# Kernel optimization log

Measured on AMD Instinct MI355X. Metric: run time of the kernel, lower is better.

The kernel has to match this reference:

```python
import jax, jax.numpy as jnp
import numpy as np

ALPHA = 0.1  # LeakyReLU negative slope
F_OUT = 128

def _leaky(x):
    return jnp.where(x >= 0, x, ALPHA * x)

def setup_inputs() -> dict:
    key = jax.random.key(0)
    ks = jax.random.split(key, 12)
    B, N, F_IN = 4, 4096, 128
    q = jax.random.normal(ks[0], (B, N, F_IN), jnp.float32)
    k = jax.random.normal(ks[1], (B, N, F_IN), jnp.float32)
    v = jax.random.normal(ks[2], (B, N, F_IN), jnp.float32)
    adj = jax.random.randint(ks[3], (B, N, N), 0, 2, jnp.int32)
    s = 1.0 / np.sqrt(F_IN)
    Wq_w = jax.random.uniform(ks[4], (F_OUT, F_IN), jnp.float32, -s, s)
    Wq_b = jax.random.uniform(ks[5], (F_OUT,), jnp.float32, -s, s)
    Wk_w = jax.random.uniform(ks[6], (F_OUT, F_IN), jnp.float32, -s, s)
    Wk_b = jax.random.uniform(ks[7], (F_OUT,), jnp.float32, -s, s)
    Wv_w = jax.random.uniform(ks[8], (F_OUT, F_IN), jnp.float32, -s, s)
    Wv_b = jax.random.uniform(ks[9], (F_OUT,), jnp.float32, -s, s)
    # xavier_uniform with gain=1.414 on (2F,1)
    lim = 1.414 * np.sqrt(6.0 / (2 * F_OUT + 1))
    a = jax.random.uniform(ks[10], (2 * F_OUT, 1), jnp.float32, -lim, lim)
    so = 1.0 / np.sqrt(F_OUT)
    Wo_w = jax.random.uniform(ks[11], (F_OUT, F_OUT), jnp.float32, -so, so)
    return {"q": q, "k": k, "v": v, "adj": adj, "Wq_w": Wq_w, "Wq_b": Wq_b,
            "Wk_w": Wk_w, "Wk_b": Wk_b, "Wv_w": Wv_w, "Wv_b": Wv_b,
            "a": a, "Wo_w": Wo_w}

def reference(q, k, v, adj, Wq_w, Wq_b, Wk_w, Wk_b, Wv_w, Wv_b, a, Wo_w):
    qp = q @ Wq_w.T + Wq_b                      # (B,N,F)
    kp = k @ Wk_w.T + Wk_b
    vp = v @ Wv_w.T + Wv_b
    Wh1 = qp @ a[:F_OUT]                        # (B,N,1)
    Wh2 = kp @ a[F_OUT:]                        # (B,N,1)
    e = _leaky(Wh1 + jnp.swapaxes(Wh2, 1, 2))   # (B,N,N)
    e = jnp.where(adj > 0, e, jnp.float32(-1e9))
    att = jax.nn.softmax(e, axis=-1)
    h = jnp.einsum('bnm,bmf->bnf', att, vp)     # (B,N,F)
    return _leaky(h @ Wo_w.T)
```

## Files before the change

### kernel.cpp

```cpp
#include <hip/hip_runtime.h>


constexpr int B = 4, N = 4096, F = 128;
constexpr int BN = B * N;
constexpr int BK = 64;
constexpr int SPLITS = 4;
constexpr int JC = N / SPLITS;
constexpr int NIT = JC / BK;
#define ALPHA 0.1f

using float4v = __attribute__((ext_vector_type(4))) float;
using short8 = __attribute__((ext_vector_type(8))) short;

__device__ __forceinline__ float leaky(float x) { return x >= 0.f ? x : ALPHA * x; }
__device__ __forceinline__ unsigned short f2bf(float x) {
    unsigned u = __float_as_uint(x);
    u = (u + 0x7FFFu + ((u >> 16) & 1u)) >> 16;
    return (unsigned short)u;
}
__device__ __forceinline__ unsigned pack_bf2(float lo, float hi) {
    unsigned a = __float_as_uint(lo), b2 = __float_as_uint(hi);
    a = a + 0x7FFFu + ((a >> 16) & 1u);
    b2 = b2 + 0x7FFFu + ((b2 >> 16) & 1u);
    return __builtin_amdgcn_perm(b2, a, 0x07060302u);
}

__global__ void k_prep(const float* __restrict__ Wq_w, const float* __restrict__ Wq_b,
                       const float* __restrict__ Wk_w, const float* __restrict__ Wk_b,
                       const float* __restrict__ a, float* __restrict__ c1,
                       float* __restrict__ c2, float* __restrict__ d12) {
    __shared__ float as[2 * F];
    __shared__ float red[2 * F];
    int t = threadIdx.x;
    as[t] = a[t];
    __syncthreads();
    int f = t & 127;
    const float* W = (t < F) ? Wq_w : Wk_w;
    const float* ao = (t < F) ? as : as + F;
    float s = 0.f;
#pragma unroll 8
    for (int o = 0; o < F; o++) s = fmaf(W[o * F + f], ao[o], s);
    if (t < F) c1[f] = s; else c2[f] = s;
    red[t] = (t < F) ? Wq_b[f] * as[f] : Wk_b[f] * as[F + f];
    __syncthreads();
    for (int st = 64; st > 0; st >>= 1) {
        if (f < st) red[t] += red[t + st];
        __syncthreads();
    }
    if (t == 0) d12[0] = red[0];
    if (t == F) d12[1] = red[F];
}

__global__ void k_wh(const float* __restrict__ q, const float* __restrict__ k,
                     const float* __restrict__ c1, const float* __restrict__ c2,
                     const float* __restrict__ d12,
                     float* __restrict__ Wh1, float* __restrict__ Wh2) {
    __shared__ float c1s[F], c2s[F];
    int t = threadIdx.x;
    if (t < F) c1s[t] = c1[t]; else c2s[t - F] = c2[t - F];
    __syncthreads();
    int row = blockIdx.x * 8 + (t >> 5);
    int lane = t & 31;
    float4 q4 = reinterpret_cast<const float4*>(q)[row * 32 + lane];
    float4 k4 = reinterpret_cast<const float4*>(k)[row * 32 + lane];
    float s1 = q4.x * c1s[lane * 4 + 0] + q4.y * c1s[lane * 4 + 1] +
               q4.z * c1s[lane * 4 + 2] + q4.w * c1s[lane * 4 + 3];
    float s2 = k4.x * c2s[lane * 4 + 0] + k4.y * c2s[lane * 4 + 1] +
               k4.z * c2s[lane * 4 + 2] + k4.w * c2s[lane * 4 + 3];
    for (int m = 16; m > 0; m >>= 1) { s1 += __shfl_xor(s1, m); s2 += __shfl_xor(s2, m); }
    if (lane == 0) { Wh1[row] = s1 + d12[0]; Wh2[row] = s2 + d12[1]; }
}

__global__ void k_max2(const float* __restrict__ Wh2, float* __restrict__ M2) {
    int b = blockIdx.x, t = threadIdx.x;
    float m = -1e30f;
    for (int i = t; i < N; i += 256) m = fmaxf(m, Wh2[b * N + i]);
    __shared__ float red[256];
    red[t] = m;
    __syncthreads();
    for (int s = 128; s > 0; s >>= 1) { if (t < s) red[t] = fmaxf(red[t], red[t + s]); __syncthreads(); }
    if (t == 0) M2[b] = red[0];
}

__global__ void k_tab(const float* __restrict__ Wh1, const float* __restrict__ Wh2,
                      const float* __restrict__ M2,
                      float* __restrict__ P1, float* __restrict__ Q1,
                      float* __restrict__ P2, float* __restrict__ Q2) {
    int i = blockIdx.x * 256 + threadIdx.x;
    int b = i >> 12;
    float w1 = Wh1[i], w2 = Wh2[i];
    float mi = leaky(w1 + M2[b]);
    P1[i] = __expf(w1 - mi);
    Q1[i] = __expf(ALPHA * w1 - mi);
    P2[i] = __expf(w2);
    Q2[i] = __expf(ALPHA * w2);
}

__global__ __launch_bounds__(256) void k_vp(const float* __restrict__ v,
                                            const float* __restrict__ Wv_w,
                                            const float* __restrict__ Wv_b,
                                            unsigned short* __restrict__ vpT) {
    __shared__ float vs[32][F];
    __shared__ float Ws[F][129];
    __shared__ unsigned short ts[F][40];
    int t = threadIdx.x;
    int row0g = blockIdx.x * 32;
    int b = row0g >> 12;
    int row0 = row0g & (N - 1);
    {
        const float4* src = reinterpret_cast<const float4*>(v + row0g * F);
        float4* dst = reinterpret_cast<float4*>(&vs[0][0]);
#pragma unroll
        for (int u = 0; u < 4; u++) dst[u * 256 + t] = src[u * 256 + t];
    }
    {
        const float4* src = reinterpret_cast<const float4*>(Wv_w);
#pragma unroll
        for (int u = 0; u < 16; u++) {
            int unit = u * 256 + t;
            int r = unit >> 5, s = unit & 31;
            float4 val = src[unit];
            Ws[r][s * 4 + 0] = val.x; Ws[r][s * 4 + 1] = val.y;
            Ws[r][s * 4 + 2] = val.z; Ws[r][s * 4 + 3] = val.w;
        }
    }
    int f = t & 127, g = t >> 7;
    float bias = Wv_b[f];
    __syncthreads();
    float acc[16];
#pragma unroll
    for (int r = 0; r < 16; r++) acc[r] = bias;
    for (int kk = 0; kk < F; kk++) {
        float wk = Ws[f][kk];
#pragma unroll
        for (int r = 0; r < 16; r++) acc[r] = fmaf(vs[g * 16 + r][kk], wk, acc[r]);
    }
#pragma unroll
    for (int r = 0; r < 16; r++) ts[f][g * 16 + r] = f2bf(acc[r]);
    __syncthreads();
    int fr = t >> 1, hseg = t & 1;
    uint4 d0 = *reinterpret_cast<uint4*>(&ts[fr][hseg * 16]);
    uint4 d1 = *reinterpret_cast<uint4*>(&ts[fr][hseg * 16 + 8]);
    unsigned short* dst = vpT + ((size_t)(b * F + fr) * N + row0 + hseg * 16);
    *reinterpret_cast<uint4*>(dst) = d0;
    *reinterpret_cast<uint4*>(dst + 8) = d1;
}

__global__ __launch_bounds__(256, 2) void k_attn(
    const unsigned short* __restrict__ vpT, const int* __restrict__ adj,
    const float* __restrict__ Wh1, const float* __restrict__ P1, const float* __restrict__ Q1,
    const float* __restrict__ P2, const float* __restrict__ Q2, const float* __restrict__ Wh2,
    float* __restrict__ h_part, float* __restrict__ den_part) {
    __shared__ __align__(16) unsigned short bs[2][F][72];
    __shared__ __align__(16) float sP2[JC], sQ2[JC], sW2[JC];
    int t = threadIdx.x;
    int idx = blockIdx.x;
    int split = idx & 3;
    int tile = (idx >> 2) & 31;
    int b = idx >> 7;
    int i0 = tile * 128;
    int jb0 = split * JC;
    int widx = t >> 6, lane = t & 63, m = lane & 15, q = lane >> 4;
    int r0 = i0 + widx * 32;

    {
        reinterpret_cast<float4*>(sP2)[t] = reinterpret_cast<const float4*>(P2 + b * N + jb0)[t];
        reinterpret_cast<float4*>(sQ2)[t] = reinterpret_cast<const float4*>(Q2 + b * N + jb0)[t];
        reinterpret_cast<float4*>(sW2)[t] = reinterpret_cast<const float4*>(Wh2 + b * N + jb0)[t];
    }

    int gi0 = b * N + r0 + m;
    int gi1 = gi0 + 16;
    float p1a = P1[gi0], q1a = Q1[gi0], t1a = -Wh1[gi0];
    float p1b = P1[gi1], q1b = Q1[gi1], t1b = -Wh1[gi1];

    const unsigned short* vb = vpT + (size_t)b * F * N + jb0;
    const int* adjbase = adj + (size_t)gi0 * N + jb0 + q * 8;

    uint4 sreg[4];
    int4 aregA[8], aregB[8];

    auto load_stage = [&](int it) {
#pragma unroll
        for (int u = 0; u < 4; u++) {
            int unit = u * 256 + t;
            int r = unit >> 3, s = unit & 7;
            sreg[u] = *reinterpret_cast<const uint4*>(vb + (size_t)r * N + it * BK + s * 8);
        }
    };
    auto write_stage = [&](int pb) {
#pragma unroll
        for (int u = 0; u < 4; u++) {
            int unit = u * 256 + t;
            int r = unit >> 3, s = unit & 7;
            *reinterpret_cast<uint4*>(&bs[pb][r][s * 8]) = sreg[u];
        }
    };
    auto load_adj = [&](int it, int4* ar) {
#pragma unroll
        for (int rt = 0; rt < 2; rt++)
#pragma unroll
            for (int kh = 0; kh < 2; kh++) {
                const int* p = adjbase + (size_t)rt * 16 * N + it * BK + kh * 32;
                ar[(rt * 2 + kh) * 2 + 0] = *reinterpret_cast<const int4*>(p);
                ar[(rt * 2 + kh) * 2 + 1] = *reinterpret_cast<const int4*>(p + 4);
            }
    };

    float4v acc0[8], acc1[8];
#pragma unroll
    for (int nt = 0; nt < 8; nt++) {
        acc0[nt] = (float4v){0.f, 0.f, 0.f, 0.f};
        acc1[nt] = (float4v){0.f, 0.f, 0.f, 0.f};
    }
    float den0 = 0.f, den1 = 0.f;

    auto gen_af = [&](const int4& a0, const int4& a1, const float4& x2a, const float4& x2b,
                      const float4& p2a, const float4& p2b, const float4& q2a, const float4& q2b,
                      float p1, float q1, float t1, float& den) -> short8 {
        float w0 = a0.x ? ((x2a.x >= t1) ? p1 * p2a.x : q1 * q2a.x) : 0.f;
        float w1 = a0.y ? ((x2a.y >= t1) ? p1 * p2a.y : q1 * q2a.y) : 0.f;
        float w2 = a0.z ? ((x2a.z >= t1) ? p1 * p2a.z : q1 * q2a.z) : 0.f;
        float w3 = a0.w ? ((x2a.w >= t1) ? p1 * p2a.w : q1 * q2a.w) : 0.f;
        float w4 = a1.x ? ((x2b.x >= t1) ? p1 * p2b.x : q1 * q2b.x) : 0.f;
        float w5 = a1.y ? ((x2b.y >= t1) ? p1 * p2b.y : q1 * q2b.y) : 0.f;
        float w6 = a1.z ? ((x2b.z >= t1) ? p1 * p2b.z : q1 * q2b.z) : 0.f;
        float w7 = a1.w ? ((x2b.w >= t1) ? p1 * p2b.w : q1 * q2b.w) : 0.f;
        den += ((w0 + w1) + (w2 + w3)) + ((w4 + w5) + (w6 + w7));
        union { short8 s; uint4 u; } r;
        r.u.x = pack_bf2(w0, w1); r.u.y = pack_bf2(w2, w3);
        r.u.z = pack_bf2(w4, w5); r.u.w = pack_bf2(w6, w7);
        return r.s;
    };

    auto body = [&](int it, int4* cur, int4* nxt, int pb) {
        if (it + 1 < NIT) {
            load_stage(it + 1);
            load_adj(it + 1, nxt);
        }
#pragma unroll
        for (int kh = 0; kh < 2; kh++) {
            int jl = it * BK + kh * 32 + q * 8;
            float4 x2a = *reinterpret_cast<const float4*>(&sW2[jl]);
            float4 x2b = *reinterpret_cast<const float4*>(&sW2[jl + 4]);
            float4 p2a = *reinterpret_cast<const float4*>(&sP2[jl]);
            float4 p2b = *reinterpret_cast<const float4*>(&sP2[jl + 4]);
            float4 q2a = *reinterpret_cast<const float4*>(&sQ2[jl]);
            float4 q2b = *reinterpret_cast<const float4*>(&sQ2[jl + 4]);
            short8 af0 = gen_af(cur[kh * 2 + 0], cur[kh * 2 + 1], x2a, x2b, p2a, p2b, q2a, q2b,
                                p1a, q1a, t1a, den0);
            short8 af1 = gen_af(cur[(2 + kh) * 2 + 0], cur[(2 + kh) * 2 + 1], x2a, x2b, p2a, p2b,
                                q2a, q2b, p1b, q1b, t1b, den1);
#pragma unroll
            for (int nt = 0; nt < 8; nt++) {
                short8 bf = *reinterpret_cast<const short8*>(&bs[pb][nt * 16 + m][kh * 32 + q * 8]);
                acc0[nt] = __builtin_amdgcn_mfma_f32_16x16x32_bf16(af0, bf, acc0[nt], 0, 0, 0);
                acc1[nt] = __builtin_amdgcn_mfma_f32_16x16x32_bf16(af1, bf, acc1[nt], 0, 0, 0);
            }
        }
        if (it + 1 < NIT) write_stage(pb ^ 1);
        __syncthreads();
    };

    load_stage(0);
    load_adj(0, aregA);
    write_stage(0);
    __syncthreads();

#pragma unroll 1
    for (int ith = 0; ith < NIT / 2; ith++) {
        body(ith * 2 + 0, aregA, aregB, 0);
        body(ith * 2 + 1, aregB, aregA, 1);
    }

    den0 += __shfl_xor(den0, 16); den0 += __shfl_xor(den0, 32);
    den1 += __shfl_xor(den1, 16); den1 += __shfl_xor(den1, 32);
    float* dp = den_part + (size_t)split * BN;
    if (q == 0) { dp[gi0] = den0; dp[gi1] = den1; }
    float* hp = h_part + (size_t)split * BN * F;
    int orow0 = b * N + r0 + q * 4;
#pragma unroll
    for (int nt = 0; nt < 8; nt++)
#pragma unroll
        for (int r = 0; r < 4; r++) {
            hp[(size_t)(orow0 + r) * F + nt * 16 + m] = acc0[nt][r];
            hp[(size_t)(orow0 + 16 + r) * F + nt * 16 + m] = acc1[nt][r];
        }
}

__global__ __launch_bounds__(256) void k_out(const float* __restrict__ h_part,
                                             const float* __restrict__ den_part,
                                             const float* __restrict__ Wo_w,
                                             float* __restrict__ out) {
    __shared__ float hs[32][F];
    __shared__ float Ws[F][129];
    int t = threadIdx.x;
    int row0 = blockIdx.x * 32;
    {
        const float4* src = reinterpret_cast<const float4*>(Wo_w);
#pragma unroll
        for (int u = 0; u < 16; u++) {
            int unit = u * 256 + t;
            int r = unit >> 5, s = unit & 31;
            float4 val = src[unit];
            Ws[r][s * 4 + 0] = val.x; Ws[r][s * 4 + 1] = val.y;
            Ws[r][s * 4 + 2] = val.z; Ws[r][s * 4 + 3] = val.w;
        }
    }
#pragma unroll
    for (int u = 0; u < 4; u++) {
        int unit = u * 256 + t;
        int r = unit >> 5, s = unit & 31;
        size_t off = (size_t)(row0 + r) * F + s * 4;
        float4 h0 = *reinterpret_cast<const float4*>(h_part + off);
        float4 h1 = *reinterpret_cast<const float4*>(h_part + (size_t)BN * F + off);
        float4 h2 = *reinterpret_cast<const float4*>(h_part + (size_t)2 * BN * F + off);
        float4 h3 = *reinterpret_cast<const float4*>(h_part + (size_t)3 * BN * F + off);
        float dsum = den_part[row0 + r] + den_part[BN + row0 + r] +
                     den_part[2 * BN + row0 + r] + den_part[3 * BN + row0 + r];
        float inv = 1.f / dsum;
        hs[r][s * 4 + 0] = (h0.x + h1.x + h2.x + h3.x) * inv;
        hs[r][s * 4 + 1] = (h0.y + h1.y + h2.y + h3.y) * inv;
        hs[r][s * 4 + 2] = (h0.z + h1.z + h2.z + h3.z) * inv;
        hs[r][s * 4 + 3] = (h0.w + h1.w + h2.w + h3.w) * inv;
    }
    __syncthreads();
    int f = t & 127, g = t >> 7;
    float acc[16];
#pragma unroll
    for (int r = 0; r < 16; r++) acc[r] = 0.f;
    for (int kk = 0; kk < F; kk++) {
        float wk = Ws[f][kk];
#pragma unroll
        for (int r = 0; r < 16; r++) acc[r] = fmaf(hs[g * 16 + r][kk], wk, acc[r]);
    }
#pragma unroll
    for (int r = 0; r < 16; r++) out[(size_t)(row0 + g * 16 + r) * F + f] = leaky(acc[r]);
}

extern "C" void kernel_launch(void* const* d_in, const int* in_sizes, int n_in,
                              void* d_out, int out_size, void* d_ws, size_t ws_size,
                              hipStream_t stream) {
    const float* q    = (const float*)d_in[0];
    const float* k    = (const float*)d_in[1];
    const float* v    = (const float*)d_in[2];
    const int*   adj  = (const int*)d_in[3];
    const float* Wq_w = (const float*)d_in[4];
    const float* Wq_b = (const float*)d_in[5];
    const float* Wk_w = (const float*)d_in[6];
    const float* Wk_b = (const float*)d_in[7];
    const float* Wv_w = (const float*)d_in[8];
    const float* Wv_b = (const float*)d_in[9];
    const float* a    = (const float*)d_in[10];
    const float* Wo_w = (const float*)d_in[11];
    float* out = (float*)d_out;
    float* ws = (float*)d_ws;

    unsigned short* vpT = (unsigned short*)ws;
    float* h_part   = ws + BN * F / 2;
    float* den_part = h_part + (size_t)SPLITS * BN * F;
    float* Wh1 = den_part + SPLITS * BN;
    float* Wh2 = Wh1 + BN;
    float* P1  = Wh2 + BN;
    float* Q1  = P1 + BN;
    float* P2  = Q1 + BN;
    float* Q2  = P2 + BN;
    float* c1  = Q2 + BN;
    float* c2  = c1 + F;
    float* d12 = c2 + F;
    float* M2  = d12 + 2;

    k_prep<<<1, 256, 0, stream>>>(Wq_w, Wq_b, Wk_w, Wk_b, a, c1, c2, d12);
    k_wh<<<BN / 8, 256, 0, stream>>>(q, k, c1, c2, d12, Wh1, Wh2);
    k_max2<<<B, 256, 0, stream>>>(Wh2, M2);
    k_tab<<<BN / 256, 256, 0, stream>>>(Wh1, Wh2, M2, P1, Q1, P2, Q2);
    k_vp<<<BN / 32, 256, 0, stream>>>(v, Wv_w, Wv_b, vpT);
    k_attn<<<B * 32 * SPLITS, 256, 0, stream>>>(vpT, adj, Wh1, P1, Q1, P2, Q2, Wh2,
                                                h_part, den_part);
    k_out<<<BN / 32, 256, 0, stream>>>(h_part, den_part, Wo_w, out);
}
```

Before: 508.3 us.

## Drop LDS staging of V in attention kernel and halve row tile per block

The attention kernel no longer stages the bf16 V^T tile in shared memory with double buffering and barriers. Each wave now loads its MFMA B-fragments straight from global memory (via cache) and processes 16 rows instead of 32. Blocks cover 64 rows, the grid doubles, and launch bounds ask for 4 blocks per CU to raise occupancy. The cost is that each V fragment is reused by only one row tile per wave rather than two, so global/L2 traffic for V roughly doubles and loads become strided rather than coalesced through LDS.

```diff
diff --git a/kernel.cpp b/kernel.cpp
--- a/kernel.cpp
+++ b/kernel.cpp
@@ -146,22 +146,20 @@
     *reinterpret_cast<uint4*>(dst + 8) = d1;
 }
 
-__global__ __launch_bounds__(256, 2) void k_attn(
+__global__ __launch_bounds__(256, 4) void k_attn(
     const unsigned short* __restrict__ vpT, const int* __restrict__ adj,
     const float* __restrict__ Wh1, const float* __restrict__ P1, const float* __restrict__ Q1,
     const float* __restrict__ P2, const float* __restrict__ Q2, const float* __restrict__ Wh2,
     float* __restrict__ h_part, float* __restrict__ den_part) {
-    __shared__ __align__(16) unsigned short bs[2][F][72];
     __shared__ __align__(16) float sP2[JC], sQ2[JC], sW2[JC];
     int t = threadIdx.x;
     int idx = blockIdx.x;
     int split = idx & 3;
-    int tile = (idx >> 2) & 31;
-    int b = idx >> 7;
-    int i0 = tile * 128;
+    int tile = (idx >> 2) & 63;
+    int b = idx >> 8;
+    int i0 = tile * 64;
     int jb0 = split * JC;
     int widx = t >> 6, lane = t & 63, m = lane & 15, q = lane >> 4;
-    int r0 = i0 + widx * 32;
 
     {
         reinterpret_cast<float4*>(sP2)[t] = reinterpret_cast<const float4*>(P2 + b * N + jb0)[t];
@@ -169,55 +167,33 @@
         reinterpret_cast<float4*>(sW2)[t] = reinterpret_cast<const float4*>(Wh2 + b * N + jb0)[t];
     }
 
-    int gi0 = b * N + r0 + m;
-    int gi1 = gi0 + 16;
-    float p1a = P1[gi0], q1a = Q1[gi0], t1a = -Wh1[gi0];
-    float p1b = P1[gi1], q1b = Q1[gi1], t1b = -Wh1[gi1];
-
-    const unsigned short* vb = vpT + (size_t)b * F * N + jb0;
-    const int* adjbase = adj + (size_t)gi0 * N + jb0 + q * 8;
-
-    uint4 sreg[4];
-    int4 aregA[8], aregB[8];
-
-    auto load_stage = [&](int it) {
-#pragma unroll
-        for (int u = 0; u < 4; u++) {
-            int unit = u * 256 + t;
-            int r = unit >> 3, s = unit & 7;
-            sreg[u] = *reinterpret_cast<const uint4*>(vb + (size_t)r * N + it * BK + s * 8);
+    int gi = b * N + i0 + widx * 16 + m;
+    float p1 = P1[gi], q1 = Q1[gi], t1 = -Wh1[gi];
+
+    const unsigned short* vbl = vpT + (size_t)b * F * N + (size_t)m * N + jb0 + q * 8;
+    const int* adjr = adj + (size_t)gi * N + jb0 + q * 8;
+
+    __syncthreads();
+
+    int4 aregA[4], aregB[4];
+
+    auto load_adj = [&](int it, int4* ar) {
+#pragma unroll
+        for (int kh = 0; kh < 2; kh++) {
+            const int* p = adjr + it * BK + kh * 32;
+            ar[kh * 2 + 0] = *reinterpret_cast<const int4*>(p);
+            ar[kh * 2 + 1] = *reinterpret_cast<const int4*>(p + 4);
         }
     };
-    auto write_stage = [&](int pb) {
-#pragma unroll
-        for (int u = 0; u < 4; u++) {
-            int unit = u * 256 + t;
-            int r = unit >> 3, s = unit & 7;
-            *reinterpret_cast<uint4*>(&bs[pb][r][s * 8]) = sreg[u];
-        }
-    };
-    auto load_adj = [&](int it, int4* ar) {
-#pragma unroll
-        for (int rt = 0; rt < 2; rt++)
-#pragma unroll
-            for (int kh = 0; kh < 2; kh++) {
-                const int* p = adjbase + (size_t)rt * 16 * N + it * BK + kh * 32;
-                ar[(rt * 2 + kh) * 2 + 0] = *reinterpret_cast<const int4*>(p);
-                ar[(rt * 2 + kh) * 2 + 1] = *reinterpret_cast<const int4*>(p + 4);
-            }
-    };
-
-    float4v acc0[8], acc1[8];
-#pragma unroll
-    for (int nt = 0; nt < 8; nt++) {
-        acc0[nt] = (float4v){0.f, 0.f, 0.f, 0.f};
-        acc1[nt] = (float4v){0.f, 0.f, 0.f, 0.f};
-    }
-    float den0 = 0.f, den1 = 0.f;
+
+    float4v acc[8];
+#pragma unroll
+    for (int nt = 0; nt < 8; nt++) acc[nt] = (float4v){0.f, 0.f, 0.f, 0.f};
+    float den = 0.f;
 
     auto gen_af = [&](const int4& a0, const int4& a1, const float4& x2a, const float4& x2b,
-                      const float4& p2a, const float4& p2b, const float4& q2a, const float4& q2b,
-                      float p1, float q1, float t1, float& den) -> short8 {
+                      const float4& p2a, const float4& p2b, const float4& q2a,
+                      const float4& q2b, float& dn) -> short8 {
         float w0 = a0.x ? ((x2a.x >= t1) ? p1 * p2a.x : q1 * q2a.x) : 0.f;
         float w1 = a0.y ? ((x2a.y >= t1) ? p1 * p2a.y : q1 * q2a.y) : 0.f;
         float w2 = a0.z ? ((x2a.z >= t1) ? p1 * p2a.z : q1 * q2a.z) : 0.f;
@@ -226,18 +202,15 @@
         float w5 = a1.y ? ((x2b.y >= t1) ? p1 * p2b.y : q1 * q2b.y) : 0.f;
         float w6 = a1.z ? ((x2b.z >= t1) ? p1 * p2b.z : q1 * q2b.z) : 0.f;
         float w7 = a1.w ? ((x2b.w >= t1) ? p1 * p2b.w : q1 * q2b.w) : 0.f;
-        den += ((w0 + w1) + (w2 + w3)) + ((w4 + w5) + (w6 + w7));
+        dn += ((w0 + w1) + (w2 + w3)) + ((w4 + w5) + (w6 + w7));
         union { short8 s; uint4 u; } r;
         r.u.x = pack_bf2(w0, w1); r.u.y = pack_bf2(w2, w3);
         r.u.z = pack_bf2(w4, w5); r.u.w = pack_bf2(w6, w7);
         return r.s;
     };
 
-    auto body = [&](int it, int4* cur, int4* nxt, int pb) {
-        if (it + 1 < NIT) {
-            load_stage(it + 1);
-            load_adj(it + 1, nxt);
-        }
+    auto body = [&](int it, int4* cur, int4* nxt) {
+        if (it + 1 < NIT) load_adj(it + 1, nxt);
 #pragma unroll
         for (int kh = 0; kh < 2; kh++) {
             int jl = it * BK + kh * 32 + q * 8;
@@ -247,45 +220,35 @@
             float4 p2b = *reinterpret_cast<const float4*>(&sP2[jl + 4]);
             float4 q2a = *reinterpret_cast<const float4*>(&sQ2[jl]);
             float4 q2b = *reinterpret_cast<const float4*>(&sQ2[jl + 4]);
-            short8 af0 = gen_af(cur[kh * 2 + 0], cur[kh * 2 + 1], x2a, x2b, p2a, p2b, q2a, q2b,
-                                p1a, q1a, t1a, den0);
-            short8 af1 = gen_af(cur[(2 + kh) * 2 + 0], cur[(2 + kh) * 2 + 1], x2a, x2b, p2a, p2b,
-                                q2a, q2b, p1b, q1b, t1b, den1);
+            short8 af = gen_af(cur[kh * 2 + 0], cur[kh * 2 + 1], x2a, x2b,
+                               p2a, p2b, q2a, q2b, den);
+            const unsigned short* vk = vbl + it * BK + kh * 32;
 #pragma unroll
             for (int nt = 0; nt < 8; nt++) {
-                short8 bf = *reinterpret_cast<const short8*>(&bs[pb][nt * 16 + m][kh * 32 + q * 8]);
-                acc0[nt] = __builtin_amdgcn_mfma_f32_16x16x32_bf16(af0, bf, acc0[nt], 0, 0, 0);
-                acc1[nt] = __builtin_amdgcn_mfma_f32_16x16x32_bf16(af1, bf, acc1[nt], 0, 0, 0);
+                short8 bf = *reinterpret_cast<const short8*>(vk + (size_t)nt * 16 * N);
+                acc[nt] = __builtin_amdgcn_mfma_f32_16x16x32_bf16(af, bf, acc[nt], 0, 0, 0);
             }
         }
-        if (it + 1 < NIT) write_stage(pb ^ 1);
-        __syncthreads();
     };
 
-    load_stage(0);
     load_adj(0, aregA);
-    write_stage(0);
-    __syncthreads();
-
 #pragma unroll 1
     for (int ith = 0; ith < NIT / 2; ith++) {
-        body(ith * 2 + 0, aregA, aregB, 0);
-        body(ith * 2 + 1, aregB, aregA, 1);
-    }
-
-    den0 += __shfl_xor(den0, 16); den0 += __shfl_xor(den0, 32);
-    den1 += __shfl_xor(den1, 16); den1 += __shfl_xor(den1, 32);
+        body(ith * 2 + 0, aregA, aregB);
+        body(ith * 2 + 1, aregB, aregA);
+    }
+
+    den += __shfl_xor(den, 16);
+    den += __shfl_xor(den, 32);
     float* dp = den_part + (size_t)split * BN;
-    if (q == 0) { dp[gi0] = den0; dp[gi1] = den1; }
+    if (q == 0) dp[gi] = den;
     float* hp = h_part + (size_t)split * BN * F;
-    int orow0 = b * N + r0 + q * 4;
+    int orow = b * N + i0 + widx * 16 + q * 4;
 #pragma unroll
     for (int nt = 0; nt < 8; nt++)
 #pragma unroll
-        for (int r = 0; r < 4; r++) {
-            hp[(size_t)(orow0 + r) * F + nt * 16 + m] = acc0[nt][r];
-            hp[(size_t)(orow0 + 16 + r) * F + nt * 16 + m] = acc1[nt][r];
-        }
+        for (int r = 0; r < 4; r++)
+            hp[(size_t)(orow + r) * F + nt * 16 + m] = acc[nt][r];
 }
 
 __global__ __launch_bounds__(256) void k_out(const float* __restrict__ h_part,
@@ -375,7 +338,7 @@
     k_max2<<<B, 256, 0, stream>>>(Wh2, M2);
     k_tab<<<BN / 256, 256, 0, stream>>>(Wh1, Wh2, M2, P1, Q1, P2, Q2);
     k_vp<<<BN / 32, 256, 0, stream>>>(v, Wv_w, Wv_b, vpT);
-    k_attn<<<B * 32 * SPLITS, 256, 0, stream>>>(vpT, adj, Wh1, P1, Q1, P2, Q2, Wh2,
+    k_attn<<<B * 64 * SPLITS, 256, 0, stream>>>(vpT, adj, Wh1, P1, Q1, P2, Q2, Wh2,
                                                 h_part, den_part);
     k_out<<<BN / 32, 256, 0, stream>>>(h_part, den_part, Wo_w, out);
 }
```

After: 632.6 us. 1.24x slower.
